# Kernel optimization log

Hardware: AMD Instinct MI355X
Metric: run time of the kernel (lower is better)

Reference implementation:

```python
import jax, jax.numpy as jnp
import numpy as np

# Hierarchy from the source module: super-class -> list of fine sub-classes
HIERARCHY_MAP = {0: [0, 1], 1: [2, 3, 4, 5, 6, 7, 8], 2: [9, 10, 11, 12, 13], 3: [14, 15]}
NUM_CLASSES = 16
N = 2_097_152  # batch size; logits are 128 MB fp32
EPS = 1e-8


def setup_inputs() -> dict:
    key = jax.random.key(0)
    k1, k2, k3 = jax.random.split(key, 3)
    logits = jax.random.normal(k1, (N, NUM_CLASSES), dtype=jnp.float32)
    # targets in [0, 4): valid both as fine-class indices and super-class indices
    remapped_targets = jax.random.randint(k2, (N,), 0, 4, dtype=jnp.int32)
    is_fine = jax.random.randint(k3, (N,), 0, 2, dtype=jnp.int32)  # 1 -> 'fine', 0 -> 'coarse'
    # Membership matrix M[s, c] = 1 if fine class c belongs to super class s
    mask = np.zeros((len(HIERARCHY_MAP), NUM_CLASSES), dtype=np.float32)
    for s, subs in HIERARCHY_MAP.items():
        mask[s, subs] = 1.0
    return {
        "logits": logits,
        "remapped_targets": remapped_targets,
        "is_fine": is_fine,
        "super_mask": jnp.asarray(mask),
    }


def reference(logits, remapped_targets, is_fine, super_mask):
    # log-softmax over classes, numerically stable, computed once
    log_probs = jax.nn.log_softmax(logits, axis=1)  # [N, C]
    # fine branch: -log p[target]
    fine_nll = -jnp.take_along_axis(log_probs, remapped_targets[:, None], axis=1)[:, 0]  # [N]
    # coarse branch: -log(sum_{c in subclasses(target)} p[c] + eps)
    mask_rows = super_mask[remapped_targets]  # [N, C] gather of membership rows
    coarse_nll = -jnp.log(jnp.sum(jnp.exp(log_probs) * mask_rows, axis=1) + EPS)  # [N]
    per_sample = jnp.where(is_fine == 1, fine_nll, coarse_nll)
    return jnp.mean(per_sample)
```

## Files before the change

kernel.cpp:

```cpp
#include <hip/hip_runtime.h>
#include <hip/hip_bf16.h>


#define TPB 256
#define RPT 4
#define ROWS_PER_BLOCK (TPB * RPT)

template <bool FULL>
__global__ __launch_bounds__(TPB) void hce_main(
    const float* __restrict__ logits,
    const int* __restrict__ targets,
    const int* __restrict__ is_fine,
    const float* __restrict__ super_mask,
    double* __restrict__ acc,
    int N)
{
    const int t = threadIdx.x;
    const int base = blockIdx.x * ROWS_PER_BLOCK + t;

    const float4* __restrict__ lg4 = (const float4*)logits;
    const float4* __restrict__ mk4 = (const float4*)super_mask;

    unsigned mb[4];
    #pragma unroll
    for (int s = 0; s < 4; ++s) {
        unsigned m = 0;
        #pragma unroll
        for (int q = 0; q < 4; ++q) {
            float4 v = mk4[s * 4 + q];
            m |= (v.x != 0.0f ? 1u : 0u) << (4 * q + 0);
            m |= (v.y != 0.0f ? 1u : 0u) << (4 * q + 1);
            m |= (v.z != 0.0f ? 1u : 0u) << (4 * q + 2);
            m |= (v.w != 0.0f ? 1u : 0u) << (4 * q + 3);
        }
        mb[s] = m;
    }

    float local = 0.0f;

    #pragma unroll
    for (int k = 0; k < RPT; ++k) {
        const int row = base + k * TPB;
        if (FULL || row < N) {
            float4 a = lg4[row * 4 + 0];
            float4 b = lg4[row * 4 + 1];
            float4 c = lg4[row * 4 + 2];
            float4 d = lg4[row * 4 + 3];
            const int tgt = targets[row];
            const int fin = is_fine[row];

            unsigned mcoarse = (tgt & 2) ? ((tgt & 1) ? mb[3] : mb[2])
                                         : ((tgt & 1) ? mb[1] : mb[0]);
            unsigned B = (fin == 1) ? (1u << tgt) : mcoarse;

            float e[16];
            e[0]=__expf(a.x);  e[1]=__expf(a.y);  e[2]=__expf(a.z);  e[3]=__expf(a.w);
            e[4]=__expf(b.x);  e[5]=__expf(b.y);  e[6]=__expf(b.z);  e[7]=__expf(b.w);
            e[8]=__expf(c.x);  e[9]=__expf(c.y);  e[10]=__expf(c.z); e[11]=__expf(c.w);
            e[12]=__expf(d.x); e[13]=__expf(d.y); e[14]=__expf(d.z); e[15]=__expf(d.w);

            float s = 0.0f, sel = 0.0f;
            #pragma unroll
            for (int i = 0; i < 16; ++i) {
                s += e[i];
                sel = fmaf((float)((B >> i) & 1u), e[i], sel);
            }

            local += __logf(s) - __logf(fmaf(1e-8f, s, sel));
        }
    }

    #pragma unroll
    for (int off = 1; off < 64; off <<= 1)
        local += __shfl_xor(local, off);

    __shared__ float wsum[TPB / 64];
    const int wave = t >> 6;
    if ((t & 63) == 0) wsum[wave] = local;
    __syncthreads();
    if (t == 0) {
        float blockSum = 0.0f;
        #pragma unroll
        for (int w = 0; w < TPB / 64; ++w) blockSum += wsum[w];
        atomicAdd(acc, (double)blockSum);
    }
}

__global__ void hce_finalize(const double* __restrict__ acc,
                             float* __restrict__ out, int N)
{
    out[0] = (float)(acc[0] / (double)N);
}

extern "C" void kernel_launch(void* const* d_in, const int* in_sizes, int n_in,
                              void* d_out, int out_size, void* d_ws, size_t ws_size,
                              hipStream_t stream)
{
    const float* logits     = (const float*)d_in[0];
    const int*   targets    = (const int*)d_in[1];
    const int*   is_fine    = (const int*)d_in[2];
    const float* super_mask = (const float*)d_in[3];
    float*       out        = (float*)d_out;
    double*      acc        = (double*)d_ws;

    const int N = in_sizes[1];

    hipMemsetAsync(acc, 0, sizeof(double), stream);

    const int blocks = (N + ROWS_PER_BLOCK - 1) / ROWS_PER_BLOCK;
    if (N % ROWS_PER_BLOCK == 0)
        hce_main<true><<<blocks, TPB, 0, stream>>>(logits, targets, is_fine, super_mask, acc, N);
    else
        hce_main<false><<<blocks, TPB, 0, stream>>>(logits, targets, is_fine, super_mask, acc, N);
    hce_finalize<<<1, 1, 0, stream>>>(acc, out, N);
}
```

Baseline: 212.2 us.

## Split each row across four lanes for coalesced loads and drop finalize kernel

Each row of 16 logits is now handled by four adjacent threads, each loading one float4, so a wave reads contiguous memory instead of each thread striding 64 bytes. Per-row sums are combined with quad shuffles. Block count grows fourfold. The double accumulator and finalize kernel are removed in favour of a float atomicAdd of pre-scaled block sums straight into the output, which saves a launch but lowers accumulation precision and adds many more atomics.

```diff
diff --git a/kernel.cpp b/kernel.cpp
--- a/kernel.cpp
+++ b/kernel.cpp
@@ -1,10 +1,10 @@
 #include <hip/hip_runtime.h>
-#include <hip/hip_bf16.h>
 
 
 #define TPB 256
 #define RPT 4
-#define ROWS_PER_BLOCK (TPB * RPT)
+#define RPG (TPB / 4)
+#define ROWS_PER_BLOCK (RPG * RPT)
 
 template <bool FULL>
 __global__ __launch_bounds__(TPB) void hce_main(
@@ -12,11 +12,12 @@
     const int* __restrict__ targets,
     const int* __restrict__ is_fine,
     const float* __restrict__ super_mask,
-    double* __restrict__ acc,
-    int N)
+    float* __restrict__ out,
+    int N, float invN)
 {
     const int t = threadIdx.x;
-    const int base = blockIdx.x * ROWS_PER_BLOCK + t;
+    const int q = t & 3;
+    const int g = t >> 2;
 
     const float4* __restrict__ lg4 = (const float4*)logits;
     const float4* __restrict__ mk4 = (const float4*)super_mask;
@@ -26,47 +27,47 @@
     for (int s = 0; s < 4; ++s) {
         unsigned m = 0;
         #pragma unroll
-        for (int q = 0; q < 4; ++q) {
-            float4 v = mk4[s * 4 + q];
-            m |= (v.x != 0.0f ? 1u : 0u) << (4 * q + 0);
-            m |= (v.y != 0.0f ? 1u : 0u) << (4 * q + 1);
-            m |= (v.z != 0.0f ? 1u : 0u) << (4 * q + 2);
-            m |= (v.w != 0.0f ? 1u : 0u) << (4 * q + 3);
+        for (int p = 0; p < 4; ++p) {
+            float4 v = mk4[s * 4 + p];
+            m |= (v.x != 0.0f ? 1u : 0u) << (4 * p + 0);
+            m |= (v.y != 0.0f ? 1u : 0u) << (4 * p + 1);
+            m |= (v.z != 0.0f ? 1u : 0u) << (4 * p + 2);
+            m |= (v.w != 0.0f ? 1u : 0u) << (4 * p + 3);
         }
         mb[s] = m;
     }
 
     float local = 0.0f;
+    const int rowbase = blockIdx.x * ROWS_PER_BLOCK + g;
 
     #pragma unroll
     for (int k = 0; k < RPT; ++k) {
-        const int row = base + k * TPB;
+        const int row = rowbase + k * RPG;
         if (FULL || row < N) {
-            float4 a = lg4[row * 4 + 0];
-            float4 b = lg4[row * 4 + 1];
-            float4 c = lg4[row * 4 + 2];
-            float4 d = lg4[row * 4 + 3];
+            float4 v = lg4[row * 4 + q];
             const int tgt = targets[row];
             const int fin = is_fine[row];
 
             unsigned mcoarse = (tgt & 2) ? ((tgt & 1) ? mb[3] : mb[2])
                                          : ((tgt & 1) ? mb[1] : mb[0]);
-            unsigned B = (fin == 1) ? (1u << tgt) : mcoarse;
+            unsigned B  = (fin == 1) ? (1u << tgt) : mcoarse;
+            unsigned Bq = (B >> (4 * q)) & 0xFu;
 
-            float e[16];
-            e[0]=__expf(a.x);  e[1]=__expf(a.y);  e[2]=__expf(a.z);  e[3]=__expf(a.w);
-            e[4]=__expf(b.x);  e[5]=__expf(b.y);  e[6]=__expf(b.z);  e[7]=__expf(b.w);
-            e[8]=__expf(c.x);  e[9]=__expf(c.y);  e[10]=__expf(c.z); e[11]=__expf(c.w);
-            e[12]=__expf(d.x); e[13]=__expf(d.y); e[14]=__expf(d.z); e[15]=__expf(d.w);
+            float e0 = __expf(v.x), e1 = __expf(v.y),
+                  e2 = __expf(v.z), e3 = __expf(v.w);
 
-            float s = 0.0f, sel = 0.0f;
-            #pragma unroll
-            for (int i = 0; i < 16; ++i) {
-                s += e[i];
-                sel = fmaf((float)((B >> i) & 1u), e[i], sel);
-            }
+            float s   = (e0 + e1) + (e2 + e3);
+            float sel = 0.0f;
+            sel = fmaf((float)( Bq       & 1u), e0, sel);
+            sel = fmaf((float)((Bq >> 1) & 1u), e1, sel);
+            sel = fmaf((float)((Bq >> 2) & 1u), e2, sel);
+            sel = fmaf((float)((Bq >> 3) & 1u), e3, sel);
 
-            local += __logf(s) - __logf(fmaf(1e-8f, s, sel));
+            s   += __shfl_xor(s, 1);   s   += __shfl_xor(s, 2);
+            sel += __shfl_xor(sel, 1); sel += __shfl_xor(sel, 2);
+
+            float nll = __logf(s) - __logf(fmaf(1e-8f, s, sel));
+            local += (q == 0) ? nll : 0.0f;
         }
     }
 
@@ -82,14 +83,8 @@
         float blockSum = 0.0f;
         #pragma unroll
         for (int w = 0; w < TPB / 64; ++w) blockSum += wsum[w];
-        atomicAdd(acc, (double)blockSum);
+        atomicAdd(out, blockSum * invN);
     }
-}
-
-__global__ void hce_finalize(const double* __restrict__ acc,
-                             float* __restrict__ out, int N)
-{
-    out[0] = (float)(acc[0] / (double)N);
 }
 
 extern "C" void kernel_launch(void* const* d_in, const int* in_sizes, int n_in,
@@ -101,16 +96,17 @@
     const int*   is_fine    = (const int*)d_in[2];
     const float* super_mask = (const float*)d_in[3];
     float*       out        = (float*)d_out;
-    double*      acc        = (double*)d_ws;
 
     const int N = in_sizes[1];
+    const float invN = 1.0f / (float)N;
 
-    hipMemsetAsync(acc, 0, sizeof(double), stream);
+    hipMemsetAsync(out, 0, sizeof(float), stream);
 
     const int blocks = (N + ROWS_PER_BLOCK - 1) / ROWS_PER_BLOCK;
     if (N % ROWS_PER_BLOCK == 0)
-        hce_main<true><<<blocks, TPB, 0, stream>>>(logits, targets, is_fine, super_mask, acc, N);
+        hce_main<true><<<blocks, TPB, 0, stream>>>(logits, targets, is_fine,
+                                                   super_mask, out, N, invN);
     else
-        hce_main<false><<<blocks, TPB, 0, stream>>>(logits, targets, is_fine, super_mask, acc, N);
-    hce_finalize<<<1, 1, 0, stream>>>(acc, out, N);
+        hce_main<false><<<blocks, TPB, 0, stream>>>(logits, targets, is_fine,
+                                                    super_mask, out, N, invN);
 }
```

New measurement: 267.5 us. 1.26x slower.
